# Kernel tuning notes

Measured on AMD Instinct MI355X. Metric: run time of the kernel, lower is better.

The kernel has to match this reference:

```python
import jax, jax.numpy as jnp
import numpy as np

E = 2      # expansion
G = 8      # groups
K = 128    # num_clusters
N = 1024   # feature_size (dim)
D = E * N // G  # per-group cluster dim = 256
EPS = 1e-12


def _l2norm(v, axis):
    return v / jnp.maximum(jnp.linalg.norm(v, axis=axis, keepdims=True), EPS)


def setup_inputs() -> dict:
    key = jax.random.key(0)
    ks = jax.random.split(key, 8)
    x = jax.random.normal(ks[0], (64, N, 8, 8), dtype=jnp.float32)
    W_inp = jax.random.normal(ks[1], (E * N, N), dtype=jnp.float32) * 0.02
    b_inp = jax.random.uniform(ks[2], (E * N,), dtype=jnp.float32)
    W_g = jax.random.normal(ks[3], (G, E * N), dtype=jnp.float32) * 0.02
    b_g = jax.random.uniform(ks[4], (G,), dtype=jnp.float32)
    W_gk = jax.random.normal(ks[5], (G * K, E * N), dtype=jnp.float32) * 0.02
    b_gk = jax.random.uniform(ks[6], (G * K,), dtype=jnp.float32)
    centroids = jax.random.normal(ks[7], (K, D), dtype=jnp.float32) * 0.1
    return {"x": x, "W_inp": W_inp, "b_inp": b_inp, "W_g": W_g, "b_g": b_g,
            "W_gk": W_gk, "b_gk": b_gk, "centroids": centroids}


def reference(x, W_inp, b_inp, W_g, b_g, W_gk, b_gk, centroids):
    b8, c, h, w = x.shape
    bs = b8 // 8
    # [bs*8, C, H, W] -> [bs, M=8*H*W, N=C]
    x = x.reshape(bs, 8, c, h, w).transpose(0, 2, 1, 3, 4).reshape(bs, c, 8 * h * w)
    x = jnp.transpose(x, (0, 2, 1))            # [bs, M, N]
    M = x.shape[1]
    x = _l2norm(x, axis=2)                     # normalize_input
    x = x @ W_inp.T + b_inp                    # [bs, M, E*N]
    alpha_g = jax.nn.sigmoid(x @ W_g.T + b_g)  # [bs, M, G]
    # NOTE: original uses Softmax(dim=1) -> softmax over token dim M
    alpha_gk = jax.nn.softmax(x @ W_gk.T + b_gk, axis=1)   # [bs, M, G*K]
    alpha_gk = alpha_gk.reshape(bs, M, G, K)
    xr = x.reshape(bs, M, G, D)
    w_full = alpha_g[..., None] * alpha_gk     # [bs, M, G, K]
    # vlad[b,k,d] = sum_{m,g} w*(x - c) = einsum(w,x) - (sum w) * c
    vlad = jnp.einsum('bmgk,bmgd->bkd', w_full, xr) \
        - jnp.sum(w_full, axis=(1, 2))[..., None] * centroids  # [bs, K, D]
    vlad = _l2norm(vlad, axis=-1).reshape(bs, K * D)
    return _l2norm(vlad, axis=1)
```

## Files before the change

### kernel.cpp

```cpp
#include <hip/hip_runtime.h>
#include <hip/hip_bf16.h>
#include <math.h>

#define EPSN 1e-12f
typedef unsigned short ushort_t;

typedef float f32x4 __attribute__((ext_vector_type(4)));
typedef short s16x8 __attribute__((ext_vector_type(8)));
typedef unsigned short u16x8 __attribute__((ext_vector_type(8)));
typedef unsigned short u16x4 __attribute__((ext_vector_type(4)));

__device__ __forceinline__ void gload_lds16(const void* g, void* l) {
  __builtin_amdgcn_global_load_lds((const __attribute__((address_space(1))) void*)g,
                                   (__attribute__((address_space(3))) void*)l, 16, 0, 0);
}

__global__ void k0_ssq(const float* __restrict__ x, float* __restrict__ ssq8) {
  int b8 = blockIdx.x >> 3;
  int cc = blockIdx.x & 7;
  int t = threadIdx.x;
  int s4 = (t & 15) * 4;
  int cg = t >> 4;
  const float* xp = x + (size_t)b8 * 65536 + (size_t)cc * 128 * 64;
  float4 a = {0.f, 0.f, 0.f, 0.f};
#pragma unroll
  for (int j = 0; j < 8; ++j) {
    int c = cg + j * 16;
    float4 v = *(const float4*)(xp + (size_t)c * 64 + s4);
    a.x = fmaf(v.x, v.x, a.x);
    a.y = fmaf(v.y, v.y, a.y);
    a.z = fmaf(v.z, v.z, a.z);
    a.w = fmaf(v.w, v.w, a.w);
  }
  __shared__ float red[16][68];
  *(float4*)&red[cg][s4] = a;
  __syncthreads();
  if (t < 64) {
    float s = 0.f;
#pragma unroll
    for (int g = 0; g < 16; ++g) s += red[g][t];
    ssq8[cc * 4096 + b8 * 64 + t] = s;
  }
}

__global__ void k1_transpose(const float* __restrict__ x, const float* __restrict__ ssq8,
                             __hip_bfloat16* __restrict__ xnb) {
  int ct = blockIdx.x;
  int b8 = blockIdx.y;
  int t = threadIdx.x;
  __shared__ float tile[64][65];
  __shared__ float ivs[64];
  if (t < 64) {
    float s = 0.f;
#pragma unroll
    for (int cc = 0; cc < 8; ++cc) s += ssq8[cc * 4096 + b8 * 64 + t];
    ivs[t] = rsqrtf(fmaxf(s, 1e-24f));
  }
  int s = t & 63, cq = t >> 6;
  const float* xp = x + (size_t)b8 * 65536 + (size_t)ct * 64 * 64;
#pragma unroll
  for (int r = 0; r < 16; ++r) {
    int cl = cq * 16 + r;
    tile[cl][s] = xp[cl * 64 + s];
  }
  __syncthreads();
  int cl = t & 63, sq = t >> 6;
#pragma unroll
  for (int r = 0; r < 16; ++r) {
    int smm = sq * 16 + r;
    int tm = b8 * 64 + smm;
    xnb[(size_t)tm * 1024 + ct * 64 + cl] = __float2bfloat16(tile[cl][smm] * ivs[smm]);
  }
}

__global__ void kpack2(const float* __restrict__ Wi, const float* __restrict__ Wgk,
                       const float* __restrict__ W_g, const float* __restrict__ b_inp,
                       const float* __restrict__ b_g, __hip_bfloat16* __restrict__ oWi,
                       __hip_bfloat16* __restrict__ oWx, ushort_t* __restrict__ oWibT,
                       float* __restrict__ bWg) {
  int bid = blockIdx.x;
  int t = threadIdx.x;
  if (bid < 2048) {
    int i = (bid * 256 + t) * 4;
    float4 v = *(const float4*)(Wi + i);
    oWi[i + 0] = __float2bfloat16(v.x);
    oWi[i + 1] = __float2bfloat16(v.y);
    oWi[i + 2] = __float2bfloat16(v.z);
    oWi[i + 3] = __float2bfloat16(v.w);
  } else if (bid < 4096) {
    int i = ((bid - 2048) * 256 + t) * 4;
    float4 v = *(const float4*)(Wgk + i);
    oWx[i + 0] = __float2bfloat16(v.x);
    oWx[i + 1] = __float2bfloat16(v.y);
    oWx[i + 2] = __float2bfloat16(v.z);
    oWx[i + 3] = __float2bfloat16(v.w);
  } else if (bid < 4112) {
    int i = (bid - 4096) * 1024 + t * 4;
    float4 v = *(const float4*)(W_g + i);
    __hip_bfloat16* o = oWx + 1024 * 2048 + i;
    o[0] = __float2bfloat16(v.x);
    o[1] = __float2bfloat16(v.y);
    o[2] = __float2bfloat16(v.z);
    o[3] = __float2bfloat16(v.w);
  } else if (bid < 4352) {
    int i = (bid - 4112) * 1024 + t * 4;
    ushort_t* o = (ushort_t*)(oWx + 1032 * 2048) + i;
    *(u16x4*)o = (u16x4){0, 0, 0, 0};
  } else if (bid < 4360) {
    int j = bid - 4352;
    const float* row = W_g + (size_t)j * 2048;
    float s = 0.f;
    for (int c = t; c < 2048; c += 256) s = fmaf(b_inp[c], row[c], s);
    __shared__ float red[256];
    red[t] = s;
    __syncthreads();
    for (int o = 128; o > 0; o >>= 1) {
      if (t < o) red[t] += red[t + o];
      __syncthreads();
    }
    if (t == 0) bWg[j] = red[0] + b_g[j];
  } else if (bid < 4872) {
    int tt = bid - 4360;
    int cp0 = (tt >> 4) * 64;
    int c0 = (tt & 15) * 64;
    __shared__ ushort_t tile[64][72];
    int r = t >> 2, cs = (t & 3) * 16;
    const float* src = Wi + (size_t)(cp0 + r) * 1024 + c0 + cs;
#pragma unroll
    for (int j = 0; j < 16; j += 4) {
      float4 v = *(const float4*)(src + j);
      __hip_bfloat16 h0 = __float2bfloat16(v.x), h1 = __float2bfloat16(v.y);
      __hip_bfloat16 h2 = __float2bfloat16(v.z), h3 = __float2bfloat16(v.w);
      tile[r][cs + j + 0] = *(ushort_t*)&h0;
      tile[r][cs + j + 1] = *(ushort_t*)&h1;
      tile[r][cs + j + 2] = *(ushort_t*)&h2;
      tile[r][cs + j + 3] = *(ushort_t*)&h3;
    }
    __syncthreads();
    int c = t >> 2, ms = (t & 3) * 16;
    u16x8 o0, o1;
#pragma unroll
    for (int j = 0; j < 8; ++j) o0[j] = tile[ms + j][c];
#pragma unroll
    for (int j = 0; j < 8; ++j) o1[j] = tile[ms + 8 + j][c];
    ushort_t* dst = oWibT + (size_t)(c0 + c) * 2048 + cp0 + ms;
    *(u16x8*)dst = o0;
    *(u16x8*)(dst + 8) = o1;
  } else {
    int i = (bid - 4872) * 1024 + t * 4;
    ushort_t* o = (ushort_t*)oWi + (size_t)3200 * 1024 + i;
    *(u16x4*)o = (u16x4){0, 0, 0, 0};
  }
}

__launch_bounds__(512, 4)
__global__ void gemm0_splitk(const ushort_t* __restrict__ A, const ushort_t* __restrict__ B,
                             float* __restrict__ Cf) {
  const int Kstride = 2048, N = 1024;
  __shared__ alignas(16) ushort_t SH[32768];
  const int tid = threadIdx.x;
  const int m0 = blockIdx.y * 128, n0 = blockIdx.x * 128;
  const int s = blockIdx.z;
  const int koff = s * 512;
  const int w = tid >> 6, l = tid & 63;
  const int wr = w >> 2, wc = w & 3;
  const int srow = w * 8 + (l >> 3);
  const int ksw = ((l & 7) ^ (l >> 3)) * 8;
  const ushort_t* Ag0 = A + (size_t)(m0 + srow) * Kstride + ksw + koff;
  const ushort_t* Ag1 = A + (size_t)(m0 + 64 + srow) * Kstride + ksw + koff;
  const ushort_t* Bg0 = B + (size_t)(n0 + srow) * Kstride + ksw + koff;
  const ushort_t* Bg1 = B + (size_t)(n0 + 64 + srow) * Kstride + ksw + koff;
  const int l0 = w * 512;
  const int l1 = 4096 + w * 512;

  f32x4 acc[4][2];
#pragma unroll
  for (int i = 0; i < 4; ++i)
#pragma unroll
    for (int j = 0; j < 2; ++j) acc[i][j] = (f32x4){0.f, 0.f, 0.f, 0.f};

  const int sw = l & 7, qq = l >> 4;

#define ASH(buf) (SH + (buf)*8192)
#define BSH(buf) (SH + 16384 + (buf)*8192)
#define STAGE(buf, k0)                               \
  {                                                  \
    gload_lds16(Ag0 + (k0), ASH(buf) + l0);          \
    gload_lds16(Ag1 + (k0), ASH(buf) + l1);          \
    gload_lds16(Bg0 + (k0), BSH(buf) + l0);          \
    gload_lds16(Bg1 + (k0), BSH(buf) + l1);          \
  }
#define COMPUTE(buf)                                                                     \
  {                                                                                      \
    s16x8 af[4][2], bf[2][2];                                                            \
    _Pragma("unroll") for (int kk = 0; kk < 2; ++kk) {                                   \
      int slot = (((kk << 2) + qq) ^ sw) * 8;                                            \
      _Pragma("unroll") for (int mi = 0; mi < 4; ++mi)                                   \
          af[mi][kk] = *(const s16x8*)&ASH(buf)[(wr * 64 + mi * 16 + (l & 15)) * 64 +    \
                                               slot];                                   \
      _Pragma("unroll") for (int ni = 0; ni < 2; ++ni)                                   \
          bf[ni][kk] = *(const s16x8*)&BSH(buf)[(wc * 32 + ni * 16 + (l & 15)) * 64 +    \
                                               slot];                                   \
    }                                                                                    \
    _Pragma("unroll") for (int kk = 0; kk < 2; ++kk)                                     \
        _Pragma("unroll") for (int mi = 0; mi < 4; ++mi)                                 \
            _Pragma("unroll") for (int ni = 0; ni < 2; ++ni)                             \
                acc[mi][ni] = __builtin_amdgcn_mfma_f32_16x16x32_bf16(af[mi][kk],        \
                                                                     bf[ni][kk],        \
                                                                     acc[mi][ni], 0, 0, 0); \
  }

  STAGE(0, 0);
  int buf = 0;
  for (int t = 0; t < 7; ++t) {
    STAGE(buf ^ 1, (t + 1) << 6);
    asm volatile("s_waitcnt vmcnt(4)" ::: "memory");
    __builtin_amdgcn_s_barrier();
    asm volatile("" ::: "memory");
    COMPUTE(buf);
    asm volatile("" ::: "memory");
    __builtin_amdgcn_s_barrier();
    buf ^= 1;
  }
  asm volatile("s_waitcnt vmcnt(0)" ::: "memory");
  __builtin_amdgcn_s_barrier();
  asm volatile("" ::: "memory");
  COMPUTE(buf);
#undef STAGE
#undef COMPUTE
#undef ASH
#undef BSH

  float* Co = Cf + (size_t)s * 1152 * 1024;
#pragma unroll
  for (int mi = 0; mi < 4; ++mi) {
    int row = m0 + wr * 64 + mi * 16 + (l >> 4) * 4;
#pragma unroll
    for (int ni = 0; ni < 2; ++ni) {
      int col = n0 + wc * 32 + ni * 16 + (l & 15);
#pragma unroll
      for (int r = 0; r < 4; ++r)
        Co[(size_t)(row + r) * N + col] = acc[mi][ni][r];
    }
  }
}

__global__ void kpackC(const float* __restrict__ Wc4, ushort_t* __restrict__ dst) {
  int i = (blockIdx.x * 256 + threadIdx.x) * 4;
  float4 a = *(const float4*)(Wc4 + i);
  float4 b = *(const float4*)(Wc4 + 1179648 + i);
  float4 c = *(const float4*)(Wc4 + 2359296 + i);
  float4 d = *(const float4*)(Wc4 + 3538944 + i);
  float4 sv = {a.x + b.x + c.x + d.x, a.y + b.y + c.y + d.y,
               a.z + b.z + c.z + d.z, a.w + b.w + c.w + d.w};
  u16x4 o;
  __hip_bfloat16 h0 = __float2bfloat16(sv.x), h1 = __float2bfloat16(sv.y);
  __hip_bfloat16 h2 = __float2bfloat16(sv.z), h3 = __float2bfloat16(sv.w);
  o[0] = *(ushort_t*)&h0; o[1] = *(ushort_t*)&h1;
  o[2] = *(ushort_t*)&h2; o[3] = *(ushort_t*)&h3;
  *(u16x4*)(dst + i) = o;
}

__launch_bounds__(512, 2)
__global__ void gemm256(const ushort_t* __restrict__ A, const ushort_t* __restrict__ B,
                        ushort_t* __restrict__ C, int K, int N) {
  __shared__ alignas(16) ushort_t SH[65536];
  const int tid = threadIdx.x;
  const int m0 = blockIdx.y * 256, n0 = blockIdx.x * 256;
  const int w = tid >> 6, l = tid & 63;
  const int wr = w >> 2, wc = w & 3;
  const int srow = w * 8 + (l >> 3);
  const int ksw = ((l & 7) ^ (l >> 3)) * 8;
  const ushort_t* Ag[4];
  const ushort_t* Bg[4];
#pragma unroll
  for (int p = 0; p < 4; ++p) {
    Ag[p] = A + (size_t)(m0 + p * 64 + srow) * K + ksw;
    Bg[p] = B + (size_t)(n0 + p * 64 + srow) * K + ksw;
  }
  const int ldst = w * 512;

  f32x4 acc[8][4];
#pragma unroll
  for (int i = 0; i < 8; ++i)
#pragma unroll
    for (int j = 0; j < 4; ++j) acc[i][j] = (f32x4){0.f, 0.f, 0.f, 0.f};

  const int sw = l & 7, qq = l >> 4;

#define ABASE(buf) (SH + (buf)*16384)
#define BBASE(buf) (SH + 32768 + (buf)*16384)
#define STAGE(buf, k0)                                           \
  {                                                              \
    _Pragma("unroll") for (int p = 0; p < 4; ++p)                \
        gload_lds16(Ag[p] + (k0), ABASE(buf) + p * 4096 + ldst); \
    _Pragma("unroll") for (int p = 0; p < 4; ++p)                \
        gload_lds16(Bg[p] + (k0), BBASE(buf) + p * 4096 + ldst); \
  }

#define COMPUTE(buf)                                                                      \
  {                                                                                       \
    const ushort_t* As = ABASE(buf);                                                      \
    const ushort_t* Bs = BBASE(buf);                                                      \
    _Pragma("unroll") for (int kk = 0; kk < 2; ++kk) {                                    \
      int slot = (((kk << 2) + qq) ^ sw) * 8;                                             \
      s16x8 bfr[4];                                                                       \
      _Pragma("unroll") for (int ni = 0; ni < 4; ++ni)                                    \
          bfr[ni] = *(const s16x8*)&Bs[(wc * 64 + ni * 16 + (l & 15)) * 64 + slot];       \
      _Pragma("unroll") for (int mi = 0; mi < 8; ++mi) {                                  \
        s16x8 a = *(const s16x8*)&As[(wr * 128 + mi * 16 + (l & 15)) * 64 + slot];        \
        _Pragma("unroll") for (int ni = 0; ni < 4; ++ni)                                  \
            acc[mi][ni] = __builtin_amdgcn_mfma_f32_16x16x32_bf16(a, bfr[ni],             \
                                                                 acc[mi][ni], 0, 0, 0);  \
      }                                                                                   \
    }                                                                                     \
  }

  const int nt = K >> 6;
  STAGE(0, 0);
  int buf = 0;
  for (int t = 0; t < nt - 1; ++t) {
    STAGE(buf ^ 1, (t + 1) << 6);
    asm volatile("s_waitcnt vmcnt(8)" ::: "memory");
    __builtin_amdgcn_s_barrier();
    asm volatile("" ::: "memory");
    COMPUTE(buf);
    asm volatile("" ::: "memory");
    __builtin_amdgcn_s_barrier();
    buf ^= 1;
  }
  asm volatile("s_waitcnt vmcnt(0)" ::: "memory");
  __builtin_amdgcn_s_barrier();
  asm volatile("" ::: "memory");
  COMPUTE(buf);
#undef STAGE
#undef COMPUTE
#undef ABASE
#undef BBASE

#pragma unroll
  for (int mi = 0; mi < 8; ++mi) {
    int row = m0 + wr * 128 + mi * 16 + (l >> 4) * 4;
#pragma unroll
    for (int ni = 0; ni < 4; ++ni) {
      int col = n0 + wc * 64 + ni * 16 + (l & 15);
#pragma unroll
      for (int r = 0; r < 4; ++r) {
        __hip_bfloat16 hb = __float2bfloat16(acc[mi][ni][r]);
        C[(size_t)(row + r) * N + col] = *(ushort_t*)&hb;
      }
    }
  }
}

__launch_bounds__(256)
__global__ void k5_softmax(const ushort_t* __restrict__ logitsTb, const float* __restrict__ bWg,
                           float* __restrict__ colsumW, ushort_t* __restrict__ wbT) {
  int wv = (blockIdx.x << 2) + (threadIdx.x >> 6);
  int q = wv >> 3, b = wv & 7;
  int l = threadIdx.x & 63;
  int g = q >> 7;
  size_t base = (size_t)q * 4096 + b * 512 + l * 8;
  u16x8 v8 = *(const u16x8*)(logitsTb + base);
  float vs[8];
#pragma unroll
  for (int i = 0; i < 8; ++i) vs[i] = __uint_as_float(((unsigned)v8[i]) << 16);
  float M = vs[0];
#pragma unroll
  for (int i = 1; i < 8; ++i) M = fmaxf(M, vs[i]);
#pragma unroll
  for (int m = 1; m < 64; m <<= 1) M = fmaxf(M, __shfl_xor(M, m, 64));
  float e[8], S = 0.f;
#pragma unroll
  for (int i = 0; i < 8; ++i) {
    e[i] = expf(vs[i] - M);
    S += e[i];
  }
#pragma unroll
  for (int m = 1; m < 64; m <<= 1) S += __shfl_xor(S, m, 64);
  float R = 1.0f / S;
  u16x8 g8 = *(const u16x8*)(logitsTb + (size_t)(1024 + g) * 4096 + b * 512 + l * 8);
  float bg = bWg[g];
  float wv8[8], wsum = 0.f;
#pragma unroll
  for (int i = 0; i < 8; ++i) {
    float gl = __uint_as_float(((unsigned)g8[i]) << 16);
    float ag = 1.0f / (1.0f + expf(-(gl + bg)));
    wv8[i] = e[i] * R * ag;
    wsum += wv8[i];
  }
#pragma unroll
  for (int m = 1; m < 64; m <<= 1) wsum += __shfl_xor(wsum, m, 64);
  if (l == 0) colsumW[b * 1024 + q] = wsum;
  u16x8 o;
#pragma unroll
  for (int i = 0; i < 8; ++i) {
    __hip_bfloat16 hb = __float2bfloat16(wv8[i]);
    o[i] = *(ushort_t*)&hb;
  }
  *(u16x8*)(wbT + base) = o;
}

__launch_bounds__(256)
__global__ void k6_vlad_mfma(const ushort_t* __restrict__ wbT, const ushort_t* __restrict__ YcT,
                             float* __restrict__ vpart) {
  int kt = blockIdx.x >> 2, dt = blockIdx.x & 3;
  int ms = blockIdx.y, b = blockIdx.z;
  __shared__ alignas(16) ushort_t Ash[2][4096];
  __shared__ alignas(16) ushort_t Bsh[2][4096];
  const int tid = threadIdx.x;
  const int w = tid >> 6, l = tid & 63;
  const int wr = w >> 1, wc = w & 1;
  const int crow = l >> 3;
  const int ksw = ((l & 7) ^ crow) * 8;

  const ushort_t* Ap[2];
  const ushort_t* Bp[2];
  int loff[2];
#pragma unroll
  for (int c = 0; c < 2; ++c) {
    int chunk = w * 2 + c;
    Ap[c] = wbT + (size_t)(kt * 64 + chunk * 8 + crow) * 4096 + b * 512 + ms * 64 + ksw;
    Bp[c] = YcT + (size_t)(dt * 64 + chunk * 8 + crow) * 4096 + b * 512 + ms * 64 + ksw;
    loff[c] = chunk * 512;
  }

  f32x4 acc[2][2];
#pragma unroll
  for (int i = 0; i < 2; ++i)
#pragma unroll
    for (int j = 0; j < 2; ++j) acc[i][j] = (f32x4){0.f, 0.f, 0.f, 0.f};

  const int sw = l & 7, qq = l >> 4;

#define STAGE6(buf, g)                                                       \
  {                                                                          \
    size_t offA = (size_t)(g)*524288;                                        \
    size_t offB = (size_t)(g)*1048576;                                       \
    gload_lds16(Ap[0] + offA, &Ash[buf][loff[0]]);                           \
    gload_lds16(Ap[1] + offA, &Ash[buf][loff[1]]);                           \
    gload_lds16(Bp[0] + offB, &Bsh[buf][loff[0]]);                           \
    gload_lds16(Bp[1] + offB, &Bsh[buf][loff[1]]);                           \
  }
#define COMPUTE6(buf)                                                                    \
  {                                                                                      \
    s16x8 af[2][2], bf[2][2];                                                            \
    _Pragma("unroll") for (int kk = 0; kk < 2; ++kk) {                                   \
      int slot = (((kk << 2) + qq) ^ sw) * 8;                                            \
      _Pragma("unroll") for (int mi = 0; mi < 2; ++mi) {                                 \
        af[mi][kk] = *(const s16x8*)&Ash[buf][(wr * 32 + mi * 16 + (l & 15)) * 64 +      \
                                             slot];                                     \
        bf[mi][kk] = *(const s16x8*)&Bsh[buf][(wc * 32 + mi * 16 + (l & 15)) * 64 +      \
                                             slot];                                     \
      }                                                                                  \
    }                                                                                    \
    _Pragma("unroll") for (int kk = 0; kk < 2; ++kk)                                     \
        _Pragma("unroll") for (int mi = 0; mi < 2; ++mi)                                 \
            _Pragma("unroll") for (int ni = 0; ni < 2; ++ni)                             \
                acc[mi][ni] = __builtin_amdgcn_mfma_f32_16x16x32_bf16(af[mi][kk],        \
                                                                     bf[ni][kk],        \
                                                                     acc[mi][ni], 0, 0, 0); \
  }

  STAGE6(0, 0);
  int buf = 0;
  for (int s = 0; s < 7; ++s) {
    STAGE6(buf ^ 1, s + 1);
    asm volatile("s_waitcnt vmcnt(4)" ::: "memory");
    __builtin_amdgcn_s_barrier();
    asm volatile("" ::: "memory");
    COMPUTE6(buf);
    asm volatile("" ::: "memory");
    __builtin_amdgcn_s_barrier();
    buf ^= 1;
  }
  asm volatile("s_waitcnt vmcnt(0)" ::: "memory");
  __builtin_amdgcn_s_barrier();
  asm volatile("" ::: "memory");
  COMPUTE6(buf);
#undef STAGE6
#undef COMPUTE6

#pragma unroll
  for (int mi = 0; mi < 2; ++mi) {
    int row = kt * 64 + wr * 32 + mi * 16 + (l >> 4) * 4;
#pragma unroll
    for (int ni = 0; ni < 2; ++ni) {
      int col = dt * 64 + wc * 32 + ni * 16 + (l & 15);
#pragma unroll
      for (int r = 0; r < 4; ++r)
        vpart[((size_t)(ms * 8 + b) * 128 + row + r) * 256 + col] = acc[mi][ni][r];
    }
  }
}

__global__ void k7_intranorm(const float* __restrict__ vpart, const float* __restrict__ colsumW,
                             const float* __restrict__ b_inp, const float* __restrict__ cent,
                             float* __restrict__ out, float* __restrict__ ss1) {
  int k = blockIdx.x;
  int b = blockIdx.y;
  int d = threadIdx.x;
  float S = 0.f, bp = 0.f;
#pragma unroll
  for (int g = 0; g < 8; ++g) {
    float cw = colsumW[b * 1024 + g * 128 + k];
    S += cw;
    bp = fmaf(b_inp[g * 256 + d], cw, bp);
  }
  size_t off = ((size_t)b * 128 + k) * 256 + d;
  float v = bp - S * cent[(size_t)k * 256 + d];
#pragma unroll
  for (int i = 0; i < 8; ++i) v += vpart[off + (size_t)i * 262144];
  float ss = v * v;
#pragma unroll
  for (int m = 1; m < 64; m <<= 1) ss += __shfl_xor(ss, m, 64);
  __shared__ float red[4];
  int lane = d & 63, wv = d >> 6;
  if (lane == 0) red[wv] = ss;
  __syncthreads();
  float tot = red[0] + red[1] + red[2] + red[3];
  float rinv = 1.0f / fmaxf(sqrtf(tot), EPSN);
  out[off] = v * rinv;
  if (d == 0) ss1[b * 128 + k] = tot * rinv * rinv;
}

__global__ void k8_finalnorm(const float* __restrict__ ss1, float* __restrict__ out) {
  int b = blockIdx.x;
  int t = threadIdx.x;
  __shared__ float red[256];
  red[t] = (t < 128) ? ss1[b * 128 + t] : 0.f;
  __syncthreads();
  for (int o = 128; o > 0; o >>= 1) {
    if (t < o) red[t] += red[t + o];
    __syncthreads();
  }
  float rinv = 1.0f / fmaxf(sqrtf(red[0]), EPSN);
  float* op = out + (size_t)b * 32768;
  for (int i = t; i < 32768; i += 256) op[i] *= rinv;
}

extern "C" void kernel_launch(void* const* d_in, const int* in_sizes, int n_in,
                              void* d_out, int out_size, void* d_ws, size_t ws_size,
                              hipStream_t stream) {
  const float* x     = (const float*)d_in[0];
  const float* W_inp = (const float*)d_in[1];
  const float* b_inp = (const float*)d_in[2];
  const float* W_g   = (const float*)d_in[3];
  const float* b_g   = (const float*)d_in[4];
  const float* W_gk  = (const float*)d_in[5];
  const float* cent  = (const float*)d_in[7];
  float* out = (float*)d_out;
  float* ws = (float*)d_ws;

  float* ssq8    = ws + 0;
  float* colsumW = ws + 32768;
  float* ss1     = ws + 40960;
  float* bWg     = ws + 41984;
  ushort_t* xnb  = (ushort_t*)(ws + 42048);
  ushort_t* wbT  = xnb;
  ushort_t* stackedA = (ushort_t*)(ws + 2139200);
  ushort_t* WibT = (ushort_t*)(ws + 3843136);
  ushort_t* Wgkx = (ushort_t*)(ws + 4891712);
  float* vpart   = ws + 3843136;
  float* Wc4     = ws + 6071360;
  ushort_t* Cstacked = (ushort_t*)(ws + 6071360);
  ushort_t* YcT      = Cstacked;
  ushort_t* logitsTb = Cstacked + (size_t)2048 * 4096;

  k0_ssq<<<512, 256, 0, stream>>>(x, ssq8);
  k1_transpose<<<dim3(16, 64), 256, 0, stream>>>(x, ssq8, (__hip_bfloat16*)xnb);
  kpack2<<<5000, 256, 0, stream>>>(W_inp, W_gk, W_g, b_inp, b_g,
                                   (__hip_bfloat16*)stackedA, (__hip_bfloat16*)Wgkx, WibT, bWg);
  gemm0_splitk<<<dim3(8, 9, 4), 512, 0, stream>>>(Wgkx, WibT, Wc4);
  kpackC<<<1152, 256, 0, stream>>>(Wc4, stackedA + (size_t)2048 * 1024);
  gemm256<<<dim3(16, 13), 512, 0, stream>>>(stackedA, xnb, Cstacked, 1024, 4096);
  k5_softmax<<<2048, 256, 0, stream>>>(logitsTb, bWg, colsumW, wbT);
  k6_vlad_mfma<<<dim3(8, 8, 8), 256, 0, stream>>>(wbT, YcT, vpart);
  k7_intranorm<<<dim3(128, 8), 256, 0, stream>>>(vpart, colsumW, b_inp, cent, out, ss1);
  k8_finalnorm<<<8, 256, 0, stream>>>(ss1, out);
}
```

Before: 119.4 us.

## Restructure main bf16 GEMM into an 8-phase pipelined loop with sub-tile staging

Rewrites the 256x256 GEMM main loop as eight phases per two K-tiles. Each phase reads a quarter sub-tile of A and B fragments from LDS, issues the next half-tile global-to-LDS load, then runs 16 MFMAs under raised wave priority. The global load layout is remapped so each half-tile can be staged on its own, with vmcnt waits placed only every fourth phase. The aim is finer interleaving of memory traffic with MFMA work, at the cost of more barriers per K-step.

Measured after the change: 122.9 us. +2.9%, slower.

```diff
diff --git a/kernel.cpp b/kernel.cpp
--- a/kernel.cpp
+++ b/kernel.cpp
@@ -262,23 +262,25 @@
 }
 
 __launch_bounds__(512, 2)
-__global__ void gemm256(const ushort_t* __restrict__ A, const ushort_t* __restrict__ B,
-                        ushort_t* __restrict__ C, int K, int N) {
+__global__ void gemm256_8ph(const ushort_t* __restrict__ A, const ushort_t* __restrict__ B,
+                            ushort_t* __restrict__ C, int K, int N) {
   __shared__ alignas(16) ushort_t SH[65536];
   const int tid = threadIdx.x;
   const int m0 = blockIdx.y * 256, n0 = blockIdx.x * 256;
   const int w = tid >> 6, l = tid & 63;
   const int wr = w >> 2, wc = w & 3;
-  const int srow = w * 8 + (l >> 3);
-  const int ksw = ((l & 7) ^ (l >> 3)) * 8;
-  const ushort_t* Ag[4];
-  const ushort_t* Bg[4];
-#pragma unroll
-  for (int p = 0; p < 4; ++p) {
-    Ag[p] = A + (size_t)(m0 + p * 64 + srow) * K + ksw;
-    Bg[p] = B + (size_t)(n0 + p * 64 + srow) * K + ksw;
-  }
-  const int ldst = w * 512;
+  const int r16 = l & 15, qq = l >> 4, sw = l & 7;
+  const int s = tid >> 3;
+  const int s_hi = s >> 5, s_lo = s & 31;
+  const int ksw = ((tid & 7) ^ (s & 7)) * 8;
+  const int NT = K >> 6;
+
+  const ushort_t* pA0 = A + (size_t)(m0 + s) * K + ksw;
+  const ushort_t* pA1 = A + (size_t)(m0 + 128 + s) * K + ksw;
+  const ushort_t* pB0 = B + (size_t)(n0 + s_hi * 64 + s_lo) * K + ksw;
+  const ushort_t* pB1 = B + (size_t)(n0 + 128 + s_hi * 64 + s_lo) * K + ksw;
+  ushort_t* dA = SH + tid * 8;
+  ushort_t* dB = SH + 32768 + tid * 8;
 
   f32x4 acc[8][4];
 #pragma unroll
@@ -286,64 +288,80 @@
 #pragma unroll
     for (int j = 0; j < 4; ++j) acc[i][j] = (f32x4){0.f, 0.f, 0.f, 0.f};
 
-  const int sw = l & 7, qq = l >> 4;
-
-#define ABASE(buf) (SH + (buf)*16384)
-#define BBASE(buf) (SH + 32768 + (buf)*16384)
-#define STAGE(buf, k0)                                           \
-  {                                                              \
-    _Pragma("unroll") for (int p = 0; p < 4; ++p)                \
-        gload_lds16(Ag[p] + (k0), ABASE(buf) + p * 4096 + ldst); \
-    _Pragma("unroll") for (int p = 0; p < 4; ++p)                \
-        gload_lds16(Bg[p] + (k0), BBASE(buf) + p * 4096 + ldst); \
-  }
-
-#define COMPUTE(buf)                                                                      \
-  {                                                                                       \
-    const ushort_t* As = ABASE(buf);                                                      \
-    const ushort_t* Bs = BBASE(buf);                                                      \
-    _Pragma("unroll") for (int kk = 0; kk < 2; ++kk) {                                    \
-      int slot = (((kk << 2) + qq) ^ sw) * 8;                                             \
-      s16x8 bfr[4];                                                                       \
-      _Pragma("unroll") for (int ni = 0; ni < 4; ++ni)                                    \
-          bfr[ni] = *(const s16x8*)&Bs[(wc * 64 + ni * 16 + (l & 15)) * 64 + slot];       \
-      _Pragma("unroll") for (int mi = 0; mi < 8; ++mi) {                                  \
-        s16x8 a = *(const s16x8*)&As[(wr * 128 + mi * 16 + (l & 15)) * 64 + slot];        \
-        _Pragma("unroll") for (int ni = 0; ni < 4; ++ni)                                  \
-            acc[mi][ni] = __builtin_amdgcn_mfma_f32_16x16x32_bf16(a, bfr[ni],             \
-                                                                 acc[mi][ni], 0, 0, 0);  \
-      }                                                                                   \
-    }                                                                                     \
-  }
-
-  const int nt = K >> 6;
-  STAGE(0, 0);
-  int buf = 0;
-  for (int t = 0; t < nt - 1; ++t) {
-    STAGE(buf ^ 1, (t + 1) << 6);
-    asm volatile("s_waitcnt vmcnt(8)" ::: "memory");
-    __builtin_amdgcn_s_barrier();
-    asm volatile("" ::: "memory");
-    COMPUTE(buf);
-    asm volatile("" ::: "memory");
-    __builtin_amdgcn_s_barrier();
-    buf ^= 1;
-  }
-  asm volatile("s_waitcnt vmcnt(0)" ::: "memory");
+#define SA(kt, h)                                                                        \
+  {                                                                                      \
+    gload_lds16(pA0 + (size_t)(h) * (K << 6) + ((kt) << 6),                              \
+                dA + (((kt)&1) << 14) + ((h) << 13));                                    \
+    gload_lds16(pA1 + (size_t)(h) * (K << 6) + ((kt) << 6),                              \
+                dA + (((kt)&1) << 14) + ((h) << 13) + 4096);                             \
+  }
+#define SB(kt, h)                                                                        \
+  {                                                                                      \
+    gload_lds16(pB0 + (size_t)(h) * (K << 5) + ((kt) << 6),                              \
+                dB + (((kt)&1) << 14) + ((h) << 13));                                    \
+    gload_lds16(pB1 + (size_t)(h) * (K << 5) + ((kt) << 6),                              \
+                dB + (((kt)&1) << 14) + ((h) << 13) + 4096);                             \
+  }
+#define VMC4 asm volatile("s_waitcnt vmcnt(4)" ::: "memory")
+
+#define PHASE(d, mh, nh, STG, VM)                                                        \
+  {                                                                                      \
+    s16x8 af[2][4], bf[2][2];                                                            \
+    _Pragma("unroll") for (int kk = 0; kk < 2; ++kk) {                                   \
+      int slot = (((kk << 2) + qq) ^ sw) * 8;                                            \
+      _Pragma("unroll") for (int ni2 = 0; ni2 < 2; ++ni2)                                \
+          bf[kk][ni2] = *(const s16x8*)&SH[32768 + ((d) << 14) + ((nh) << 13) +          \
+                                           (wc * 32 + ni2 * 16 + r16) * 64 + slot];      \
+      _Pragma("unroll") for (int mi2 = 0; mi2 < 4; ++mi2)                                \
+          af[kk][mi2] = *(const s16x8*)&SH[((d) << 14) + ((mh) << 13) +                  \
+                                           (wr * 64 + mi2 * 16 + r16) * 64 + slot];      \
+    }                                                                                    \
+    STG;                                                                                 \
+    asm volatile("" ::: "memory");                                                       \
+    __builtin_amdgcn_s_barrier();                                                        \
+    asm volatile("" ::: "memory");                                                       \
+    __builtin_amdgcn_s_setprio(1);                                                       \
+    _Pragma("unroll") for (int kk = 0; kk < 2; ++kk)                                     \
+        _Pragma("unroll") for (int mi2 = 0; mi2 < 4; ++mi2)                              \
+            _Pragma("unroll") for (int ni2 = 0; ni2 < 2; ++ni2)                          \
+                acc[(mh)*4 + mi2][(nh)*2 + ni2] = __builtin_amdgcn_mfma_f32_16x16x32_bf16( \
+                    af[kk][mi2], bf[kk][ni2], acc[(mh)*4 + mi2][(nh)*2 + ni2], 0, 0, 0); \
+    __builtin_amdgcn_s_setprio(0);                                                       \
+    VM;                                                                                  \
+    asm volatile("" ::: "memory");                                                       \
+    __builtin_amdgcn_s_barrier();                                                        \
+    asm volatile("" ::: "memory");                                                       \
+  }
+
+  SA(0, 0); SB(0, 0); SA(0, 1); SB(0, 1); SA(1, 0); SB(1, 0);
+  VMC4;
   __builtin_amdgcn_s_barrier();
   asm volatile("" ::: "memory");
-  COMPUTE(buf);
-#undef STAGE
-#undef COMPUTE
-#undef ABASE
-#undef BBASE
+
+#pragma unroll 1
+  for (int I = 0; I < (NT >> 1); ++I) {
+    const int kt = 2 * I;
+    const int k1 = kt + 1, k2 = kt + 2, k3 = kt + 3;
+    PHASE(0, 0, 0, SA(k1, 1), );
+    PHASE(0, 0, 1, SB(k1, 1), );
+    PHASE(0, 1, 0, if (k2 < NT) SA(k2, 0), );
+    PHASE(0, 1, 1, if (k2 < NT) SB(k2, 0), VMC4);
+    PHASE(1, 0, 0, if (k2 < NT) SA(k2, 1), );
+    PHASE(1, 0, 1, if (k2 < NT) SB(k2, 1), );
+    PHASE(1, 1, 0, if (k3 < NT) SA(k3, 0), );
+    PHASE(1, 1, 1, if (k3 < NT) SB(k3, 0), VMC4);
+  }
+#undef PHASE
+#undef SA
+#undef SB
+#undef VMC4
 
 #pragma unroll
   for (int mi = 0; mi < 8; ++mi) {
     int row = m0 + wr * 128 + mi * 16 + (l >> 4) * 4;
 #pragma unroll
     for (int ni = 0; ni < 4; ++ni) {
-      int col = n0 + wc * 64 + ni * 16 + (l & 15);
+      int col = n0 + wc * 64 + ni * 16 + r16;
 #pragma unroll
       for (int r = 0; r < 4; ++r) {
         __hip_bfloat16 hb = __float2bfloat16(acc[mi][ni][r]);
@@ -573,7 +591,7 @@
                                    (__hip_bfloat16*)stackedA, (__hip_bfloat16*)Wgkx, WibT, bWg);
   gemm0_splitk<<<dim3(8, 9, 4), 512, 0, stream>>>(Wgkx, WibT, Wc4);
   kpackC<<<1152, 256, 0, stream>>>(Wc4, stackedA + (size_t)2048 * 1024);
-  gemm256<<<dim3(16, 13), 512, 0, stream>>>(stackedA, xnb, Cstacked, 1024, 4096);
+  gemm256_8ph<<<dim3(16, 13), 512, 0, stream>>>(stackedA, xnb, Cstacked, 1024, 4096);
   k5_softmax<<<2048, 256, 0, stream>>>(logitsTb, bWg, colsumW, wbT);
   k6_vlad_mfma<<<dim3(8, 8, 8), 256, 0, stream>>>(wbT, YcT, vpart);
   k7_intranorm<<<dim3(128, 8), 256, 0, stream>>>(vpart, colsumW, b_inp, cent, out, ss1);
```
